# Kernel optimization log

Hardware: AMD Instinct MI355X
Metric: run time of the kernel (lower is better)

## Reference

```python
import jax, jax.numpy as jnp
import numpy as np

I = 1024
H = 1024
B = 4096
EPS = 1e-5

def layer_norm(x, gamma, beta):
    mu = jnp.mean(x, axis=-1, keepdims=True)
    var = jnp.var(x, axis=-1, keepdims=True)
    return (x - mu) * jax.lax.rsqrt(var + EPS) * gamma + beta

def setup_inputs() -> dict:
    key = jax.random.key(0)
    ks = jax.random.split(key, 5)
    return {
        "input": jax.random.normal(ks[0], (B, I), dtype=jnp.float32),
        "hx": jax.random.normal(ks[1], (B, H), dtype=jnp.float32),
        "cx": jax.random.normal(ks[2], (B, H), dtype=jnp.float32),
        "weight_ih": jax.random.normal(ks[3], (4 * H, I), dtype=jnp.float32),
        "weight_hh": jax.random.normal(ks[4], (4 * H, H), dtype=jnp.float32),
        "gamma_i": jnp.ones((4 * H,), jnp.float32),
        "beta_i": jnp.zeros((4 * H,), jnp.float32),
        "gamma_h": jnp.ones((4 * H,), jnp.float32),
        "beta_h": jnp.zeros((4 * H,), jnp.float32),
        "gamma_c": jnp.ones((H,), jnp.float32),
        "beta_c": jnp.zeros((H,), jnp.float32),
    }

def reference(input, hx, cx, weight_ih, weight_hh,
              gamma_i, beta_i, gamma_h, beta_h, gamma_c, beta_c):
    # igates: [B, 4H]
    igates = layer_norm(jnp.dot(input, weight_ih.T), gamma_i, beta_i)
    hgates = layer_norm(jnp.dot(hx, weight_hh.T), gamma_h, beta_h)
    gates = igates + hgates
    ingate, forgetgate, cellgate, outgate = jnp.split(gates, 4, axis=1)
    ingate = jax.nn.sigmoid(ingate)
    forgetgate = jax.nn.sigmoid(forgetgate)
    cellgate = jnp.tanh(cellgate)
    outgate = jax.nn.sigmoid(outgate)
    cy = layer_norm(forgetgate * cx + ingate * cellgate, gamma_c, beta_c)
    hy = outgate * jnp.tanh(cy)
    return (hy, hy, cy)
```

## Files before the change

### kernel.cpp

```cpp
#include <hip/hip_runtime.h>

#define EPS 1e-5f

typedef unsigned short u16;
typedef __attribute__((ext_vector_type(8))) __bf16 bf16x8;
typedef __attribute__((ext_vector_type(4))) float f32x4;
typedef __attribute__((ext_vector_type(8))) unsigned short ushort8;

__device__ inline float bf2f(u16 h) {
  union { unsigned u; float f; } x; x.u = ((unsigned)h) << 16; return x.f;
}
__device__ inline u16 f2bf(float f) {
  union { float f; unsigned u; } x; x.f = f;
  unsigned r = x.u + 0x7fffu + ((x.u >> 16) & 1u);
  return (u16)(r >> 16);
}
__device__ inline float sigmoidf(float x) { return 1.0f / (1.0f + __expf(-x)); }

__global__ __launch_bounds__(256) void cast4_f32_bf16(
    const float* __restrict__ s0, const float* __restrict__ s1,
    const float* __restrict__ s2, const float* __restrict__ s3,
    u16* __restrict__ d0, u16* __restrict__ d1,
    u16* __restrict__ d2, u16* __restrict__ d3, int n)
{
  const float* s = (blockIdx.y == 0) ? s0 : (blockIdx.y == 1) ? s1 : (blockIdx.y == 2) ? s2 : s3;
  u16*         d = (blockIdx.y == 0) ? d0 : (blockIdx.y == 1) ? d1 : (blockIdx.y == 2) ? d2 : d3;
  int i = (blockIdx.x * 256 + threadIdx.x) * 8;
  if (i >= n) return;
  float4 a = *(const float4*)(s + i);
  float4 b = *(const float4*)(s + i + 4);
  ushort8 o;
  o[0] = f2bf(a.x); o[1] = f2bf(a.y); o[2] = f2bf(a.z); o[3] = f2bf(a.w);
  o[4] = f2bf(b.x); o[5] = f2bf(b.y); o[6] = f2bf(b.z); o[7] = f2bf(b.w);
  *(ushort8*)(d + i) = o;
}

#define MFMA_ __builtin_amdgcn_mfma_f32_16x16x32_bf16
#define ASG __attribute__((address_space(1)))
#define ASL __attribute__((address_space(3)))

#define GLL(p, lds) __builtin_amdgcn_global_load_lds( \
    (const ASG void*)(p), (ASL void*)(lds), 16, 0, 0);

#define STAGE(nx, kt) { \
  GLL(gA0 + (kt), &sA[nx][(      tid) * 8]) \
  GLL(gA1 + (kt), &sA[nx][(256 + tid) * 8]) \
  GLL(gA2 + (kt), &sA[nx][(512 + tid) * 8]) \
  GLL(gA3 + (kt), &sA[nx][(768 + tid) * 8]) \
  GLL(gB0 + (kt), &sB[nx][(      tid) * 8]) \
  GLL(gB1 + (kt), &sB[nx][(256 + tid) * 8]) }

#define LDA(mi) (*(const bf16x8*)&sa[(arow + (mi) * 16) * 32 + k8e])
#define LDB(ni) (*(const bf16x8*)&sb[(brow + (ni) * 16) * 32 + k8e])

#define CTILE { \
  bf16x8 qf0 = LDB(0), qf1 = LDB(1), qf2 = LDB(2), qf3 = LDB(3); \
  bf16x8 af[8]; \
  _Pragma("unroll") for (int mi = 0; mi < 8; ++mi) af[mi] = LDA(mi); \
  __builtin_amdgcn_s_setprio(1); \
  _Pragma("unroll") for (int mi = 0; mi < 8; ++mi) { \
    acc[mi][0] = MFMA_(af[mi], qf0, acc[mi][0], 0, 0, 0); \
    acc[mi][1] = MFMA_(af[mi], qf1, acc[mi][1], 0, 0, 0); \
    acc[mi][2] = MFMA_(af[mi], qf2, acc[mi][2], 0, 0, 0); \
    acc[mi][3] = MFMA_(af[mi], qf3, acc[mi][3], 0, 0, 0); \
  } \
  __builtin_amdgcn_s_setprio(0); }

__global__ __launch_bounds__(256, 2) void gemm256x128_dual(
    const u16* __restrict__ A0, const u16* __restrict__ W0, u16* __restrict__ C0,
    const u16* __restrict__ A1, const u16* __restrict__ W1, u16* __restrict__ C1)
{
  constexpr int K = 1024, N = 4096, NT = 32;

  __shared__ __attribute__((aligned(16))) u16 sA[2][256 * 32];
  __shared__ __attribute__((aligned(16))) u16 sB[2][128 * 32];

  const int b0  = blockIdx.x;
  const int bid = (b0 & 7) * 128 + (b0 >> 3);

  const u16* A  = (bid < 512) ? A0 : A1;
  const u16* Wm = (bid < 512) ? W0 : W1;
  u16*       C  = (bid < 512) ? C0 : C1;
  const int b2 = bid & 511;
  const int bm = (b2 >> 5) << 8;
  const int bn = (b2 & 31) << 7;

  const int tid = threadIdx.x;
  const int l  = tid & 63;
  const int w  = tid >> 6;
  const int wr = w >> 1;
  const int wc = w & 1;

  const int r0 = tid >> 2;
  const int sc = (tid & 3) * 8;
  const u16* gA0 = A  + (size_t)(bm + r0) * K + sc;
  const u16* gA1 = gA0 + (size_t)64  * K;
  const u16* gA2 = gA0 + (size_t)128 * K;
  const u16* gA3 = gA0 + (size_t)192 * K;
  const u16* gB0 = Wm + (size_t)(bn + r0) * K + sc;
  const u16* gB1 = gB0 + (size_t)64 * K;

  const int arow = wr * 128 + (l & 15);
  const int brow = wc * 64 + (l & 15);
  const int k8e  = (l >> 4) * 8;

  f32x4 acc[8][4];
#pragma unroll
  for (int i = 0; i < 8; ++i)
#pragma unroll
    for (int j = 0; j < 4; ++j) acc[i][j] = (f32x4){0.f, 0.f, 0.f, 0.f};

  STAGE(0, 0)

  for (int t = 0; t < NT - 1; ++t) {
    const int cur = t & 1, nxt = cur ^ 1;
    STAGE(nxt, (t + 1) * 32)
    asm volatile("s_waitcnt vmcnt(6)" ::: "memory");
    __builtin_amdgcn_s_barrier();
    const u16* sa = sA[cur];
    const u16* sb = sB[cur];
    CTILE
    __builtin_amdgcn_s_barrier();
  }

  {
    asm volatile("s_waitcnt vmcnt(0)" ::: "memory");
    __builtin_amdgcn_s_barrier();
    const u16* sa = sA[1];
    const u16* sb = sB[1];
    CTILE
  }

  const int ccol = bn + wc * 64 + (l & 15);
  const int crow = bm + wr * 128 + (l >> 4) * 4;
#pragma unroll
  for (int mi = 0; mi < 8; ++mi) {
#pragma unroll
    for (int ni = 0; ni < 4; ++ni) {
      int col = ccol + ni * 16;
#pragma unroll
      for (int r = 0; r < 4; ++r) {
        int row = crow + mi * 16 + r;
        C[(size_t)row * N + col] = f2bf(acc[mi][ni][r]);
      }
    }
  }
}

__global__ __launch_bounds__(256) void lstm_epilogue(
    const u16* __restrict__ ig, const u16* __restrict__ hg,
    const float* __restrict__ cx,
    const float* __restrict__ gi, const float* __restrict__ bi,
    const float* __restrict__ gh, const float* __restrict__ bh,
    const float* __restrict__ gc, const float* __restrict__ bc,
    float* __restrict__ out)
{
  const int b = blockIdx.x;
  const int t = threadIdx.x;
  const u16* igr = ig + (size_t)b * 4096;
  const u16* hgr = hg + (size_t)b * 4096;

  __shared__ float redbuf[16];

  float iv[16], hv[16];
  float s_i = 0.f, q_i = 0.f, s_h = 0.f, q_h = 0.f;
#pragma unroll
  for (int i = 0; i < 16; ++i) {
    float a = bf2f(igr[t + 256 * i]);
    float c = bf2f(hgr[t + 256 * i]);
    iv[i] = a; hv[i] = c;
    s_i += a; q_i += a * a; s_h += c; q_h += c * c;
  }
#pragma unroll
  for (int off = 32; off > 0; off >>= 1) {
    s_i += __shfl_xor(s_i, off);
    q_i += __shfl_xor(q_i, off);
    s_h += __shfl_xor(s_h, off);
    q_h += __shfl_xor(q_h, off);
  }
  {
    int wv = t >> 6;
    if ((t & 63) == 0) {
      redbuf[wv] = s_i; redbuf[wv + 4] = q_i;
      redbuf[wv + 8] = s_h; redbuf[wv + 12] = q_h;
    }
    __syncthreads();
    s_i = redbuf[0] + redbuf[1] + redbuf[2] + redbuf[3];
    q_i = redbuf[4] + redbuf[5] + redbuf[6] + redbuf[7];
    s_h = redbuf[8] + redbuf[9] + redbuf[10] + redbuf[11];
    q_h = redbuf[12] + redbuf[13] + redbuf[14] + redbuf[15];
    __syncthreads();
  }
  const float inv4096 = 1.0f / 4096.0f;
  float mu_i = s_i * inv4096;
  float rs_i = rsqrtf(q_i * inv4096 - mu_i * mu_i + EPS);
  float mu_h = s_h * inv4096;
  float rs_h = rsqrtf(q_h * inv4096 - mu_h * mu_h + EPS);

  float c_pre[4], og[4];
  float s_c = 0.f, q_c = 0.f;
#pragma unroll
  for (int i = 0; i < 4; ++i) {
    int h = t + 256 * i;
    float g_in = ((iv[i]      - mu_i) * rs_i * gi[h]        + bi[h]) +
                 ((hv[i]      - mu_h) * rs_h * gh[h]        + bh[h]);
    float g_fg = ((iv[i + 4]  - mu_i) * rs_i * gi[h + 1024] + bi[h + 1024]) +
                 ((hv[i + 4]  - mu_h) * rs_h * gh[h + 1024] + bh[h + 1024]);
    float g_cl = ((iv[i + 8]  - mu_i) * rs_i * gi[h + 2048] + bi[h + 2048]) +
                 ((hv[i + 8]  - mu_h) * rs_h * gh[h + 2048] + bh[h + 2048]);
    float g_og = ((iv[i + 12] - mu_i) * rs_i * gi[h + 3072] + bi[h + 3072]) +
                 ((hv[i + 12] - mu_h) * rs_h * gh[h + 3072] + bh[h + 3072]);
    float in_s = sigmoidf(g_in);
    float fg_s = sigmoidf(g_fg);
    float cl_t = tanhf(g_cl);
    og[i] = sigmoidf(g_og);
    c_pre[i] = fg_s * cx[(size_t)b * 1024 + h] + in_s * cl_t;
    s_c += c_pre[i]; q_c += c_pre[i] * c_pre[i];
  }
#pragma unroll
  for (int off = 32; off > 0; off >>= 1) {
    s_c += __shfl_xor(s_c, off);
    q_c += __shfl_xor(q_c, off);
  }
  {
    int wv = t >> 6;
    if ((t & 63) == 0) { redbuf[wv] = s_c; redbuf[wv + 4] = q_c; }
    __syncthreads();
    s_c = redbuf[0] + redbuf[1] + redbuf[2] + redbuf[3];
    q_c = redbuf[4] + redbuf[5] + redbuf[6] + redbuf[7];
  }
  const float inv1024 = 1.0f / 1024.0f;
  float mu_c = s_c * inv1024;
  float rs_c = rsqrtf(q_c * inv1024 - mu_c * mu_c + EPS);

  const size_t BH = (size_t)4096 * 1024;
#pragma unroll
  for (int i = 0; i < 4; ++i) {
    int h = t + 256 * i;
    float cy = (c_pre[i] - mu_c) * rs_c * gc[h] + bc[h];
    float hy = og[i] * tanhf(cy);
    size_t o = (size_t)b * 1024 + h;
    out[o] = hy;
    out[BH + o] = hy;
    out[2 * BH + o] = cy;
  }
}

extern "C" void kernel_launch(void* const* d_in, const int* in_sizes, int n_in,
                              void* d_out, int out_size, void* d_ws, size_t ws_size,
                              hipStream_t stream) {
  const float* input = (const float*)d_in[0];
  const float* hx    = (const float*)d_in[1];
  const float* cx    = (const float*)d_in[2];
  const float* wih   = (const float*)d_in[3];
  const float* whh   = (const float*)d_in[4];
  const float* gi    = (const float*)d_in[5];
  const float* bi    = (const float*)d_in[6];
  const float* gh    = (const float*)d_in[7];
  const float* bh    = (const float*)d_in[8];
  const float* gc    = (const float*)d_in[9];
  const float* bc    = (const float*)d_in[10];
  float* out = (float*)d_out;

  char* wsp = (char*)d_ws;
  u16* a_bf  = (u16*)(wsp);
  u16* h_bf  = (u16*)(wsp + ((size_t)8  << 20));
  u16* wi_bf = (u16*)(wsp + ((size_t)16 << 20));
  u16* wh_bf = (u16*)(wsp + ((size_t)24 << 20));
  u16* ig_bf = (u16*)(wsp + ((size_t)32 << 20));
  u16* hg_bf = (u16*)(wsp + ((size_t)64 << 20));

  const int nper = 4096 * 1024;
  dim3 cgrid(nper / 8 / 256, 4);
  cast4_f32_bf16<<<cgrid, 256, 0, stream>>>(input, hx, wih, whh,
                                            a_bf, h_bf, wi_bf, wh_bf, nper);

  gemm256x128_dual<<<1024, 256, 0, stream>>>(a_bf, wi_bf, ig_bf,
                                             h_bf, wh_bf, hg_bf);

  lstm_epilogue<<<4096, 256, 0, stream>>>(ig_bf, hg_bf, cx,
                                          gi, bi, gh, bh, gc, bc, out);
}
```

Before: 130.6 us.

## Shrink GEMM tile to 128x128 with swizzled LDS and higher occupancy

Replaces the 256x128 dual GEMM tile with a 128x128 tile, doubling the grid to 2048 blocks and raising the launch-bounds occupancy target from 2 to 4 blocks per CU. It adds an XOR swizzle to the global-to-LDS store column and the LDS read slot to reduce bank conflicts, and drops the XCD-aware block remapping. The intent is better latency hiding and fewer LDS conflicts, at the cost of lower arithmetic intensity per block and more redundant global loads of A and B.

```diff
diff --git a/kernel.cpp b/kernel.cpp
--- a/kernel.cpp
+++ b/kernel.cpp
@@ -42,47 +42,51 @@
 #define GLL(p, lds) __builtin_amdgcn_global_load_lds( \
     (const ASG void*)(p), (ASL void*)(lds), 16, 0, 0);
 
-#define STAGE(nx, kt) { \
-  GLL(gA0 + (kt), &sA[nx][(      tid) * 8]) \
-  GLL(gA1 + (kt), &sA[nx][(256 + tid) * 8]) \
-  GLL(gA2 + (kt), &sA[nx][(512 + tid) * 8]) \
-  GLL(gA3 + (kt), &sA[nx][(768 + tid) * 8]) \
-  GLL(gB0 + (kt), &sB[nx][(      tid) * 8]) \
-  GLL(gB1 + (kt), &sB[nx][(256 + tid) * 8]) }
-
-#define LDA(mi) (*(const bf16x8*)&sa[(arow + (mi) * 16) * 32 + k8e])
-#define LDB(ni) (*(const bf16x8*)&sb[(brow + (ni) * 16) * 32 + k8e])
-
-#define CTILE { \
-  bf16x8 qf0 = LDB(0), qf1 = LDB(1), qf2 = LDB(2), qf3 = LDB(3); \
-  bf16x8 af[8]; \
-  _Pragma("unroll") for (int mi = 0; mi < 8; ++mi) af[mi] = LDA(mi); \
-  __builtin_amdgcn_s_setprio(1); \
-  _Pragma("unroll") for (int mi = 0; mi < 8; ++mi) { \
-    acc[mi][0] = MFMA_(af[mi], qf0, acc[mi][0], 0, 0, 0); \
-    acc[mi][1] = MFMA_(af[mi], qf1, acc[mi][1], 0, 0, 0); \
-    acc[mi][2] = MFMA_(af[mi], qf2, acc[mi][2], 0, 0, 0); \
-    acc[mi][3] = MFMA_(af[mi], qf3, acc[mi][3], 0, 0, 0); \
-  } \
-  __builtin_amdgcn_s_setprio(0); }
-
-__global__ __launch_bounds__(256, 2) void gemm256x128_dual(
+#define STAGE(nx, kn) \
+  GLL(gA_0 + (kn), &sA[nx][(      tid) * 8]) \
+  GLL(gA_1 + (kn), &sA[nx][(256 + tid) * 8]) \
+  GLL(gB_0 + (kn), &sB[nx][(      tid) * 8]) \
+  GLL(gB_1 + (kn), &sB[nx][(256 + tid) * 8])
+
+#define LDA(mi) (*(const bf16x8*)&sa[(arow + (mi) * 16) * 32 + rslot])
+#define LDB(ni) (*(const bf16x8*)&sb[(brow + (ni) * 16) * 32 + rslot])
+
+#define VMW(n) asm volatile("s_waitcnt vmcnt(" #n ")" ::: "memory");
+#define BAR __builtin_amdgcn_s_barrier();
+
+#define MFMA16 \
+  acc[0][0] = MFMA_(a0, b0, acc[0][0], 0, 0, 0); \
+  acc[0][1] = MFMA_(a0, b1, acc[0][1], 0, 0, 0); \
+  acc[0][2] = MFMA_(a0, b2, acc[0][2], 0, 0, 0); \
+  acc[0][3] = MFMA_(a0, b3, acc[0][3], 0, 0, 0); \
+  acc[1][0] = MFMA_(a1, b0, acc[1][0], 0, 0, 0); \
+  acc[1][1] = MFMA_(a1, b1, acc[1][1], 0, 0, 0); \
+  acc[1][2] = MFMA_(a1, b2, acc[1][2], 0, 0, 0); \
+  acc[1][3] = MFMA_(a1, b3, acc[1][3], 0, 0, 0); \
+  acc[2][0] = MFMA_(a2, b0, acc[2][0], 0, 0, 0); \
+  acc[2][1] = MFMA_(a2, b1, acc[2][1], 0, 0, 0); \
+  acc[2][2] = MFMA_(a2, b2, acc[2][2], 0, 0, 0); \
+  acc[2][3] = MFMA_(a2, b3, acc[2][3], 0, 0, 0); \
+  acc[3][0] = MFMA_(a3, b0, acc[3][0], 0, 0, 0); \
+  acc[3][1] = MFMA_(a3, b1, acc[3][1], 0, 0, 0); \
+  acc[3][2] = MFMA_(a3, b2, acc[3][2], 0, 0, 0); \
+  acc[3][3] = MFMA_(a3, b3, acc[3][3], 0, 0, 0);
+
+__global__ __launch_bounds__(256, 4) void gemm128_dual(
     const u16* __restrict__ A0, const u16* __restrict__ W0, u16* __restrict__ C0,
     const u16* __restrict__ A1, const u16* __restrict__ W1, u16* __restrict__ C1)
 {
   constexpr int K = 1024, N = 4096, NT = 32;
 
-  __shared__ __attribute__((aligned(16))) u16 sA[2][256 * 32];
+  __shared__ __attribute__((aligned(16))) u16 sA[2][128 * 32];
   __shared__ __attribute__((aligned(16))) u16 sB[2][128 * 32];
 
-  const int b0  = blockIdx.x;
-  const int bid = (b0 & 7) * 128 + (b0 >> 3);
-
-  const u16* A  = (bid < 512) ? A0 : A1;
-  const u16* Wm = (bid < 512) ? W0 : W1;
-  u16*       C  = (bid < 512) ? C0 : C1;
-  const int b2 = bid & 511;
-  const int bm = (b2 >> 5) << 8;
+  const int bid = blockIdx.x;
+  const u16* A  = (bid < 1024) ? A0 : A1;
+  const u16* Wm = (bid < 1024) ? W0 : W1;
+  u16*       C  = (bid < 1024) ? C0 : C1;
+  const int b2 = bid & 1023;
+  const int bm = (b2 >> 5) << 7;
   const int bn = (b2 & 31) << 7;
 
   const int tid = threadIdx.x;
@@ -91,50 +95,50 @@
   const int wr = w >> 1;
   const int wc = w & 1;
 
-  const int r0 = tid >> 2;
-  const int sc = (tid & 3) * 8;
-  const u16* gA0 = A  + (size_t)(bm + r0) * K + sc;
-  const u16* gA1 = gA0 + (size_t)64  * K;
-  const u16* gA2 = gA0 + (size_t)128 * K;
-  const u16* gA3 = gA0 + (size_t)192 * K;
-  const u16* gB0 = Wm + (size_t)(bn + r0) * K + sc;
-  const u16* gB1 = gB0 + (size_t)64 * K;
-
-  const int arow = wr * 128 + (l & 15);
+  const int srow = tid >> 2;
+  const int scol = ((tid & 3) ^ ((tid >> 3) & 3)) * 8;
+  const u16* gA_0 = A  + (size_t)(bm + srow) * K + scol;
+  const u16* gA_1 = gA_0 + (size_t)64 * K;
+  const u16* gB_0 = Wm + (size_t)(bn + srow) * K + scol;
+  const u16* gB_1 = gB_0 + (size_t)64 * K;
+
+  const int arow = wr * 64 + (l & 15);
   const int brow = wc * 64 + (l & 15);
-  const int k8e  = (l >> 4) * 8;
-
-  f32x4 acc[8][4];
-#pragma unroll
-  for (int i = 0; i < 8; ++i)
+  const int rslot = ((l >> 4) ^ ((l >> 1) & 3)) * 8;
+
+  f32x4 acc[4][4];
+#pragma unroll
+  for (int i = 0; i < 4; ++i)
 #pragma unroll
     for (int j = 0; j < 4; ++j) acc[i][j] = (f32x4){0.f, 0.f, 0.f, 0.f};
 
   STAGE(0, 0)
 
-  for (int t = 0; t < NT - 1; ++t) {
+  for (int t = 0; t < NT; ++t) {
     const int cur = t & 1, nxt = cur ^ 1;
-    STAGE(nxt, (t + 1) * 32)
-    asm volatile("s_waitcnt vmcnt(6)" ::: "memory");
-    __builtin_amdgcn_s_barrier();
     const u16* sa = sA[cur];
     const u16* sb = sB[cur];
-    CTILE
-    __builtin_amdgcn_s_barrier();
-  }
-
-  {
-    asm volatile("s_waitcnt vmcnt(0)" ::: "memory");
-    __builtin_amdgcn_s_barrier();
-    const u16* sa = sA[1];
-    const u16* sb = sB[1];
-    CTILE
+
+    if (t < NT - 1) {
+      STAGE(nxt, (t + 1) * 32)
+      VMW(4)
+    } else {
+      VMW(0)
+    }
+    BAR
+
+    bf16x8 a0, a1, a2, a3, b0, b1, b2, b3;
+    b0 = LDB(0); b1 = LDB(1); b2 = LDB(2); b3 = LDB(3);
+    a0 = LDA(0); a1 = LDA(1); a2 = LDA(2); a3 = LDA(3);
+    MFMA16
+
+    BAR
   }
 
   const int ccol = bn + wc * 64 + (l & 15);
-  const int crow = bm + wr * 128 + (l >> 4) * 4;
-#pragma unroll
-  for (int mi = 0; mi < 8; ++mi) {
+  const int crow = bm + wr * 64 + (l >> 4) * 4;
+#pragma unroll
+  for (int mi = 0; mi < 4; ++mi) {
 #pragma unroll
     for (int ni = 0; ni < 4; ++ni) {
       int col = ccol + ni * 16;
@@ -275,8 +279,8 @@
   cast4_f32_bf16<<<cgrid, 256, 0, stream>>>(input, hx, wih, whh,
                                             a_bf, h_bf, wi_bf, wh_bf, nper);
 
-  gemm256x128_dual<<<1024, 256, 0, stream>>>(a_bf, wi_bf, ig_bf,
-                                             h_bf, wh_bf, hg_bf);
+  gemm128_dual<<<2048, 256, 0, stream>>>(a_bf, wi_bf, ig_bf,
+                                         h_bf, wh_bf, hg_bf);
 
   lstm_epilogue<<<4096, 256, 0, stream>>>(ig_bf, hg_bf, cx,
                                           gi, bi, gh, bh, gc, bc, out);
```

After: 132.1 us. Within noise of the previous version (+1.1%).
